# Kernel optimization log

Hardware: AMD Instinct MI355X
Metric: run time of the kernel (lower is better)

The kernel has to match this reference:

```python
import jax, jax.numpy as jnp
import numpy as np

HIDDEN = 64
IN_DIM = 32
CONNECTION = 8
N_WARPS = (CONNECTION + 1) // 2  # range(0, connection, 2) -> 4 warps actually used


def conv2d(x, w, b, pad):
    # x: (B, Cin, H, W), w: (Cout, Cin, kh, kw)
    y = jax.lax.conv_general_dilated(
        x, w, window_strides=(1, 1), padding=[(pad, pad), (pad, pad)],
        dimension_numbers=("NCHW", "OIHW", "NCHW"))
    return y + b[None, :, None, None]


def grid_sample_bilinear(img, grid):
    """torch.nn.functional.grid_sample(mode='bilinear', padding_mode='zeros', align_corners=False).
    img: (B, C, H, W); grid: (B, H, W, 2) with grid[..., 0]=x (width), grid[..., 1]=y (height)."""
    B, C, H, W = img.shape
    gx = (grid[..., 0] + 1.0) * (W * 0.5) - 0.5  # unnormalize, align_corners=False
    gy = (grid[..., 1] + 1.0) * (H * 0.5) - 0.5
    x0 = jnp.floor(gx)
    y0 = jnp.floor(gy)
    wx1 = gx - x0
    wy1 = gy - y0
    wx0 = 1.0 - wx1
    wy0 = 1.0 - wy1

    def gather(xf, yf):
        valid = (xf >= 0) & (xf < W) & (yf >= 0) & (yf < H)
        xi = jnp.clip(xf, 0, W - 1).astype(jnp.int32)
        yi = jnp.clip(yf, 0, H - 1).astype(jnp.int32)
        # per-batch advanced gather: (C, H, W) per sample
        v = jax.vmap(lambda im, y, x: im[:, y, x])(img, yi, xi)  # (B, C, H, W)
        return v * valid[:, None, :, :].astype(img.dtype)

    out = (wy0 * wx0)[:, None] * gather(x0, y0) \
        + (wy0 * wx1)[:, None] * gather(x0 + 1, y0) \
        + (wy1 * wx0)[:, None] * gather(x0, y0 + 1) \
        + (wy1 * wx1)[:, None] * gather(x0 + 1, y0 + 1)
    return out


def setup_inputs() -> dict:
    key = jax.random.key(0)
    ks = jax.random.split(key, 10)
    B, H, W = 16, 128, 128
    s = 0.05
    return {
        "x": jax.random.normal(ks[0], (B, IN_DIM, H, W), dtype=jnp.float32),
        "h_prev": jax.random.normal(ks[1], (B, HIDDEN, H, W), dtype=jnp.float32),
        "w_in": jax.random.normal(ks[2], (3 * HIDDEN, IN_DIM, 3, 3), dtype=jnp.float32) * s,
        "b_in": jax.random.normal(ks[3], (3 * HIDDEN,), dtype=jnp.float32) * s,
        "w_proj": jax.random.normal(ks[4], (N_WARPS, 3 * HIDDEN, HIDDEN), dtype=jnp.float32) * s,
        "b_proj": jax.random.normal(ks[5], (N_WARPS, 3 * HIDDEN), dtype=jnp.float32) * s,
        "w_sub": jax.random.normal(ks[6], (2 * CONNECTION, IN_DIM + HIDDEN, 5, 5), dtype=jnp.float32) * s,
        "b_sub": jax.random.normal(ks[7], (2 * CONNECTION,), dtype=jnp.float32) * s,
    }


def reference(x, h_prev, w_in, b_in, w_proj, b_proj, w_sub, b_sub):
    d = HIDDEN
    input_conv = conv2d(x, w_in, b_in, pad=1)  # (B, 3d, H, W)
    x_z, x_r, x_h = input_conv[:, :d], input_conv[:, d:2 * d], input_conv[:, 2 * d:]

    # flow sub-network + global min-max normalization over ALL channels
    combined = jnp.concatenate([x, h_prev], axis=1)
    cc = conv2d(combined, w_sub, b_sub, pad=2)  # (B, 2*connection, H, W)
    cc = jnp.transpose(cc, (0, 2, 3, 1))        # (B, H, W, 2*connection)
    cc = (cc - cc.min()) / (cc.max() - cc.min())
    cc = 2.0 * cc - 1.0

    traj = None
    for i in range(N_WARPS):  # small fixed loop (mirrors range(0, connection, 2))
        grid = cc[..., 2 * i:2 * i + 2]
        warped = grid_sample_bilinear(h_prev, grid)  # (B, d, H, W)
        proj = jnp.einsum("bchw,oc->bohw", warped, w_proj[i]) + b_proj[i][None, :, None, None]
        traj = proj if traj is None else traj + proj

    h_z, h_r, h_h = traj[:, :d], traj[:, d:2 * d], traj[:, 2 * d:]
    z = jax.nn.sigmoid(x_z + h_z)
    r = jax.nn.sigmoid(x_r + h_r)
    h = jax.nn.leaky_relu(x_h + r * h_h, negative_slope=0.2)
    h_next = (1.0 - z) * h + z * h_prev
    return h_next
```

## Files before the change

### kernel.cpp

```cpp
#include <hip/hip_runtime.h>
#include <hip/hip_bf16.h>
#include <math.h>

#define B_    16
#define HID   64
#define CIN   32
#define OC1   192
#define CCC   16
#define HW_   128
#define NPIX  (HW_*HW_)

typedef _Float16 half8 __attribute__((ext_vector_type(8)));
typedef _Float16 half4 __attribute__((ext_vector_type(4)));
typedef float floatx4 __attribute__((ext_vector_type(4)));

__device__ __forceinline__ unsigned fenc(float f) {
    unsigned b = __float_as_uint(f);
    return (b & 0x80000000u) ? ~b : (b | 0x80000000u);
}
__device__ __forceinline__ float fdec(unsigned u) {
    unsigned b = (u & 0x80000000u) ? (u ^ 0x80000000u) : ~u;
    return __uint_as_float(b);
}

__global__ __launch_bounds__(256) void repack_kernel(
    const float* __restrict__ w_in, const float* __restrict__ w_sub,
    const float* __restrict__ w_proj, const float* __restrict__ b_proj,
    _Float16* __restrict__ wsub_f16, float* __restrict__ bsum,
    _Float16* __restrict__ win_f16, _Float16* __restrict__ wp_f16,
    unsigned* __restrict__ minmax)
{
    int idx = blockIdx.x * 256 + threadIdx.x;
    if (idx < 38400) {
        int sk = idx >> 9, r2 = idx & 511;
        int l = r2 >> 3, j = r2 & 7;
        int s = sk / 3, kc = sk - s * 3;
        int ky = s / 5, kx = s - ky * 5;
        int oc = l & 15;
        int icg = kc * 32 + (l >> 4) * 8 + j;
        wsub_f16[idx] = (_Float16)w_sub[oc * 2400 + icg * 25 + ky * 5 + kx];
    } else if (idx < 38400 + 192) {
        int o = idx - 38400;
        bsum[o] = b_proj[o] + b_proj[192 + o] + b_proj[384 + o] + b_proj[576 + o];
    } else if (idx < 38592 + 55296) {
        int j2 = idx - 38592;
        int s = j2 / 6144, r = j2 - s * 6144;
        int mt = r / 512, r2 = r - mt * 512;
        int l = r2 >> 3, j = r2 & 7;
        int oc = mt * 16 + (l & 15);
        int ic = (l >> 4) * 8 + j;
        win_f16[j2] = (_Float16)w_in[oc * 288 + ic * 9 + s];
    } else if (idx < 38592 + 55296 + 49152) {
        int j3 = idx - (38592 + 55296);
        int kt = j3 / 6144, r = j3 - kt * 6144;
        int mt = r / 512, r2 = r - mt * 512;
        int l = r2 >> 3, j = r2 & 7;
        int o = mt * 16 + (l & 15);
        int c_all = kt * 32 + (l >> 4) * 8 + j;
        int i = c_all >> 6, c = c_all & 63;
        wp_f16[j3] = (_Float16)w_proj[(i * 192 + o) * 64 + c];
    }
    if (idx == 0) { minmax[0] = 0xFFFFFFFFu; minmax[1] = 0u; }
}

__global__ __launch_bounds__(256) void transpose_h_kernel(
    const float* __restrict__ hp, const float* __restrict__ x,
    _Float16* __restrict__ hcl, _Float16* __restrict__ xcl)
{
    __shared__ float lds[64 * 129];
    int tid = threadIdx.x;
    int y = blockIdx.x, b = blockIdx.y;

    const float* hb = hp + (size_t)b * HID * NPIX + y * HW_;
#pragma unroll
    for (int it = 0; it < 32; ++it) {
        int idx = tid + it * 256;
        int c = idx >> 7, xx = idx & 127;
        lds[c * 129 + xx] = hb[(size_t)c * NPIX + xx];
    }
    __syncthreads();
    unsigned* o = (unsigned*)(hcl + (size_t)((b * HW_ + y) * HW_) * 64);
#pragma unroll
    for (int it = 0; it < 16; ++it) {
        int e2 = tid + it * 256;
        int c2 = e2 & 31, xx = e2 >> 5;
        union { _Float16 h[2]; unsigned u; } pk;
        pk.h[0] = (_Float16)lds[(c2 * 2) * 129 + xx];
        pk.h[1] = (_Float16)lds[(c2 * 2 + 1) * 129 + xx];
        o[e2] = pk.u;
    }
    __syncthreads();

    const float* xb = x + (size_t)b * CIN * NPIX + y * HW_;
#pragma unroll
    for (int it = 0; it < 16; ++it) {
        int idx = tid + it * 256;
        int c = idx >> 7, xx = idx & 127;
        lds[c * 129 + xx] = xb[(size_t)c * NPIX + xx];
    }
    __syncthreads();
    unsigned* ox = (unsigned*)(xcl + (size_t)((b * HW_ + y) * HW_) * 32);
#pragma unroll
    for (int it = 0; it < 8; ++it) {
        int e2 = tid + it * 256;
        int c2 = e2 & 15, xx = e2 >> 4;
        union { _Float16 h[2]; unsigned u; } pk;
        pk.h[0] = (_Float16)lds[(c2 * 2) * 129 + xx];
        pk.h[1] = (_Float16)lds[(c2 * 2 + 1) * 129 + xx];
        ox[e2] = pk.u;
    }
}

__global__ __launch_bounds__(256) void conv_sub_mfma(
    const _Float16* __restrict__ xcl, const _Float16* __restrict__ hcl,
    const _Float16* __restrict__ wsub_f16, const float* __restrict__ b_sub,
    float* __restrict__ cc, unsigned* __restrict__ minmax)
{
    __shared__ __align__(16) _Float16 tile[12 * 20 * 104];
    __shared__ float redmn[4], redmx[4];
    int tid = threadIdx.x;
    int b = blockIdx.z;
    int y0 = blockIdx.y * 8, x0 = blockIdx.x * 16;

#pragma unroll
    for (int it = 0; it < 8; ++it) {
        int idx = tid + it * 256;
        if (idx < 1920) {
            int yy = idx / 160, rem = idx - yy * 160;
            int px = rem >> 3, q = rem & 7;
            int gy = y0 + yy - 2, gx = x0 + px - 2;
            bool ok = ((unsigned)gy < 128u) & ((unsigned)gx < 128u);
            int cgy = min(max(gy, 0), 127), cgx = min(max(gx, 0), 127);
            uint4 v = ((const uint4*)hcl)[(size_t)((b * 128 + cgy) * 128 + cgx) * 8 + q];
            if (!ok) { v.x = 0; v.y = 0; v.z = 0; v.w = 0; }
            *(uint4*)((char*)tile + (yy * 20 + px) * 208 + 64 + q * 16) = v;
        }
    }
#pragma unroll
    for (int it = 0; it < 4; ++it) {
        int idx = tid + it * 256;
        if (idx < 960) {
            int yy = idx / 80, rem = idx - yy * 80;
            int px = rem >> 2, q = rem & 3;
            int gy = y0 + yy - 2, gx = x0 + px - 2;
            bool ok = ((unsigned)gy < 128u) & ((unsigned)gx < 128u);
            int cgy = min(max(gy, 0), 127), cgx = min(max(gx, 0), 127);
            uint4 v = ((const uint4*)xcl)[(size_t)((b * 128 + cgy) * 128 + cgx) * 4 + q];
            if (!ok) { v.x = 0; v.y = 0; v.z = 0; v.w = 0; }
            *(uint4*)((char*)tile + (yy * 20 + px) * 208 + q * 16) = v;
        }
    }
    __syncthreads();

    int w = tid >> 6, l = tid & 63;
    int quad = l >> 4, ln = l & 15;

    floatx4 sinit;
#pragma unroll
    for (int r = 0; r < 4; ++r) sinit[r] = b_sub[quad * 4 + r];
    floatx4 sacc[2] = {sinit, sinit};

#pragma unroll 5
    for (int s = 0; s < 25; ++s) {
        int ky = s / 5, kx = s - (s / 5) * 5;
#pragma unroll
        for (int kc = 0; kc < 3; ++kc) {
            half8 af = *(const half8*)(wsub_f16 + (size_t)((s * 3 + kc) * 64 + l) * 8);
#pragma unroll
            for (int t = 0; t < 2; ++t) {
                int pos = (w * 2 + t + ky) * 20 + (ln + kx);
                half8 bf = *(const half8*)(tile + pos * 104 + kc * 32 + quad * 8);
                sacc[t] = __builtin_amdgcn_mfma_f32_16x16x32_f16(af, bf, sacc[t], 0, 0, 0);
            }
        }
    }

    {
        float mn = 1e30f, mx = -1e30f;
#pragma unroll
        for (int t = 0; t < 2; ++t) {
            int yg = y0 + w * 2 + t;
#pragma unroll
            for (int r = 0; r < 4; ++r) {
                int oc = quad * 4 + r;
                float v = sacc[t][r];
                cc[((size_t)(b * CCC + oc) * HW_ + yg) * HW_ + x0 + ln] = v;
                mn = fminf(mn, v); mx = fmaxf(mx, v);
            }
        }
#pragma unroll
        for (int m = 1; m < 64; m <<= 1) {
            mn = fminf(mn, __shfl_xor(mn, m, 64));
            mx = fmaxf(mx, __shfl_xor(mx, m, 64));
        }
        if (l == 0) { redmn[w] = mn; redmx[w] = mx; }
    }
    __syncthreads();
    if (tid == 0) {
        float bmn = fminf(fminf(redmn[0], redmn[1]), fminf(redmn[2], redmn[3]));
        float bmx = fmaxf(fmaxf(redmx[0], redmx[1]), fmaxf(redmx[2], redmx[3]));
        atomicMin(&minmax[0], fenc(bmn));
        atomicMax(&minmax[1], fenc(bmx));
    }
}

__global__ __launch_bounds__(256, 3) void warp_gru_conv(
    const _Float16* __restrict__ hcl, const _Float16* __restrict__ xcl,
    const float* __restrict__ cc,
    const _Float16* __restrict__ wp_f16, const float* __restrict__ bsum,
    const _Float16* __restrict__ win_f16, const float* __restrict__ b_in,
    const unsigned* __restrict__ minmax, float* __restrict__ out)
{
    __shared__ __align__(16) _Float16 smem[64 * 256];
    _Float16* xt = smem;
    _Float16* warped = smem;
    float* ol = (float*)smem;

    int tid = threadIdx.x;
    int i = tid >> 6;
    int p = tid & 63;
    int b = blockIdx.z, y = blockIdx.y, xh = blockIdx.x;
    int xg = xh * 64 + p;
    int w = i, l = p;
    int quad = l >> 4, ln = l & 15;

    uint4 xv0, xv1, xv2, xv3;
    int xslot = -1;
    if (tid < 216) {
        int row = tid / 72, px = tid - row * 72;
        int gy = y - 1 + row, gx = xh * 64 - 4 + px;
        bool ok = ((unsigned)gy < 128u) & ((unsigned)gx < 128u);
        int cgy = min(max(gy, 0), 127), cgx = min(max(gx, 0), 127);
        const uint4* s = (const uint4*)(xcl + (size_t)((b * 128 + cgy) * 128 + cgx) * 32);
        xv0 = s[0]; xv1 = s[1]; xv2 = s[2]; xv3 = s[3];
        if (!ok) {
            xv0.x = xv0.y = xv0.z = xv0.w = 0; xv1 = xv0; xv2 = xv0; xv3 = xv0;
        }
        xslot = (row * 72 + px) * 4;
    }

    const _Float16* hclb = hcl + (size_t)b * NPIX * 64;
    half4 hpv16[4];
    {
        const _Float16* grow = hclb + (size_t)(y * HW_ + xh * 64) * 64 + 16 * w + quad * 4;
#pragma unroll
        for (int nt = 0; nt < 4; ++nt)
            hpv16[nt] = *(const half4*)(grow + (size_t)(nt * 16 + ln) * 64);
    }

    float mn = fdec(minmax[0]), mx = fdec(minmax[1]);
    float scale = 2.0f / (mx - mn);
    int ccbase = ((b * CCC + 2 * i) * HW_ + y) * HW_ + xg;
    float gxn = (cc[ccbase] - mn) * scale - 1.0f;
    float gyn = (cc[ccbase + NPIX] - mn) * scale - 1.0f;
    float gx = (gxn + 1.0f) * 64.0f - 0.5f;
    float gy = (gyn + 1.0f) * 64.0f - 0.5f;
    float x0f = floorf(gx), y0f = floorf(gy);
    float wx1 = gx - x0f, wy1 = gy - y0f;
    float wx0 = 1.0f - wx1, wy0 = 1.0f - wy1;
    int ix0 = (int)x0f, iy0 = (int)y0f;
    int ix1 = ix0 + 1, iy1 = iy0 + 1;
    bool vx0 = (unsigned)ix0 < 128u, vx1 = (unsigned)ix1 < 128u;
    bool vy0 = (unsigned)iy0 < 128u, vy1 = (unsigned)iy1 < 128u;
    _Float16 h00 = (_Float16)((vx0 && vy0) ? wy0 * wx0 : 0.f);
    _Float16 h01 = (_Float16)((vx1 && vy0) ? wy0 * wx1 : 0.f);
    _Float16 h10 = (_Float16)((vx0 && vy1) ? wy1 * wx0 : 0.f);
    _Float16 h11 = (_Float16)((vx1 && vy1) ? wy1 * wx1 : 0.f);
    int cx0 = min(max(ix0, 0), 127), cx1 = min(max(ix1, 0), 127);
    int cy0 = min(max(iy0, 0), 127), cy1 = min(max(iy1, 0), 127);

    const half8* r00 = (const half8*)(hclb + (size_t)(cy0 * HW_ + cx0) * 64);
    const half8* r01 = (const half8*)(hclb + (size_t)(cy0 * HW_ + cx1) * 64);
    const half8* r10 = (const half8*)(hclb + (size_t)(cy1 * HW_ + cx0) * 64);
    const half8* r11 = (const half8*)(hclb + (size_t)(cy1 * HW_ + cx1) * 64);

    if (xslot >= 0) {
        unsigned b0 = (unsigned)(xslot * 16);
        unsigned by0_ = b0 ^ (((b0 >> 7) & 3) << 4);
        unsigned b1 = (unsigned)((xslot + 1) * 16);
        unsigned by1_ = b1 ^ (((b1 >> 7) & 3) << 4);
        unsigned b2 = (unsigned)((xslot + 2) * 16);
        unsigned by2_ = b2 ^ (((b2 >> 7) & 3) << 4);
        unsigned b3 = (unsigned)((xslot + 3) * 16);
        unsigned by3_ = b3 ^ (((b3 >> 7) & 3) << 4);
        *(uint4*)((char*)xt + by0_) = xv0;
        *(uint4*)((char*)xt + by1_) = xv1;
        *(uint4*)((char*)xt + by2_) = xv2;
        *(uint4*)((char*)xt + by3_) = xv3;
    }
    __syncthreads();

    half8 g0[8], g1[8];
#pragma unroll
    for (int t = 0; t < 8; ++t) { g0[t] = r00[t]; g1[t] = r01[t]; }

    floatx4 accA[3][4];
    floatx4 hh[4];
#pragma unroll
    for (int t = 0; t < 2; ++t) {
        floatx4 bi = *(const floatx4*)(b_in + t * 64 + 16 * w + quad * 4);
        floatx4 bs = *(const floatx4*)(bsum + t * 64 + 16 * w + quad * 4);
        floatx4 init;
#pragma unroll
        for (int r = 0; r < 4; ++r) init[r] = bi[r] + bs[r];
#pragma unroll
        for (int nt = 0; nt < 4; ++nt) accA[t][nt] = init;
    }
    {
        floatx4 bih = *(const floatx4*)(b_in + 128 + 16 * w + quad * 4);
        floatx4 bsh = *(const floatx4*)(bsum + 128 + 16 * w + quad * 4);
#pragma unroll
        for (int nt = 0; nt < 4; ++nt) { accA[2][nt] = bih; hh[nt] = bsh; }
    }

#pragma unroll
    for (int s = 0; s < 9; ++s) {
        int ky = s / 3, kx = s - ky * 3;
        half8 af[3];
#pragma unroll
        for (int t = 0; t < 3; ++t)
            af[t] = *(const half8*)(win_f16 + (size_t)((s * 12 + (t * 4 + w)) * 64 + l) * 8);
#pragma unroll
        for (int nt = 0; nt < 4; ++nt) {
            int pxr = ky * 72 + nt * 16 + ln + kx + 3;
            unsigned byte = (unsigned)(pxr * 64 + quad * 16);
            byte ^= ((byte >> 7) & 3) << 4;
            half8 bf = *(const half8*)((char*)xt + byte);
#pragma unroll
            for (int t = 0; t < 3; ++t)
                accA[t][nt] = __builtin_amdgcn_mfma_f32_16x16x32_f16(af[t], bf, accA[t][nt], 0, 0, 0);
        }
    }
    __syncthreads();

#pragma unroll
    for (int t = 0; t < 8; ++t) {
        half8 c10 = r10[t], c11 = r11[t];
        half8 v = g0[t] * h00 + g1[t] * h01 + c10 * h10 + c11 * h11;
        int cs = (i * 8 + t) ^ (p & 7);
        *(half8*)(warped + p * 256 + cs * 8) = v;
    }
    __syncthreads();

#pragma unroll
    for (int kt = 0; kt < 8; ++kt) {
        half8 af[3];
#pragma unroll
        for (int t = 0; t < 3; ++t)
            af[t] = *(const half8*)(wp_f16 + (size_t)((kt * 12 + (t * 4 + w)) * 64 + l) * 8);
#pragma unroll
        for (int nt = 0; nt < 4; ++nt) {
            int pxi = nt * 16 + ln;
            int cs = (kt * 4 + quad) ^ (pxi & 7);
            half8 bf = *(const half8*)(warped + pxi * 256 + cs * 8);
            accA[0][nt] = __builtin_amdgcn_mfma_f32_16x16x32_f16(af[0], bf, accA[0][nt], 0, 0, 0);
            accA[1][nt] = __builtin_amdgcn_mfma_f32_16x16x32_f16(af[1], bf, accA[1][nt], 0, 0, 0);
            hh[nt]      = __builtin_amdgcn_mfma_f32_16x16x32_f16(af[2], bf, hh[nt], 0, 0, 0);
        }
    }

    float gout[4][4];
#pragma unroll
    for (int nt = 0; nt < 4; ++nt) {
#pragma unroll
        for (int r = 0; r < 4; ++r) {
            float z  = 1.0f / (1.0f + __expf(-accA[0][nt][r]));
            float rg = 1.0f / (1.0f + __expf(-accA[1][nt][r]));
            float hc = accA[2][nt][r] + rg * hh[nt][r];
            hc = hc > 0.f ? hc : 0.2f * hc;
            gout[nt][r] = (1.f - z) * hc + z * (float)hpv16[nt][r];
        }
    }

    __syncthreads();
#pragma unroll
    for (int nt = 0; nt < 4; ++nt) {
#pragma unroll
        for (int r = 0; r < 4; ++r) {
            int d = 16 * w + quad * 4 + r;
            ol[d * 68 + nt * 16 + ln] = gout[nt][r];
        }
    }
    __syncthreads();
    {
        const int pixbase = y * HW_ + xh * 64;
#pragma unroll
        for (int it = 0; it < 4; ++it) {
            int idx = tid + it * 256;
            int ch = idx >> 4, p4 = idx & 15;
            floatx4 v = *(const floatx4*)&ol[ch * 68 + p4 * 4];
            *(floatx4*)&out[(size_t)(b * HID + ch) * NPIX + pixbase + p4 * 4] = v;
        }
    }
}

extern "C" void kernel_launch(void* const* d_in, const int* in_sizes, int n_in,
                              void* d_out, int out_size, void* d_ws, size_t ws_size,
                              hipStream_t stream)
{
    const float* x      = (const float*)d_in[0];
    const float* hp     = (const float*)d_in[1];
    const float* w_in   = (const float*)d_in[2];
    const float* b_in   = (const float*)d_in[3];
    const float* w_proj = (const float*)d_in[4];
    const float* b_proj = (const float*)d_in[5];
    const float* w_sub  = (const float*)d_in[6];
    const float* b_sub  = (const float*)d_in[7];
    float* out = (float*)d_out;

    char* ws = (char*)d_ws;
    float*     ccbuf    = (float*)    ws;
    unsigned*  minmax   = (unsigned*) (ws + 16777216);
    _Float16*  wsub_f16 = (_Float16*)(ws + 16777472);
    float*     bsum     = (float*)    (ws + 16854272);
    _Float16*  win_f16  = (_Float16*)(ws + 16855296);
    _Float16*  wp_f16   = (_Float16*)(ws + 16965888);
    _Float16*  hcl16    = (_Float16*)(ws + 17064192);
    _Float16*  xcl16    = (_Float16*)(ws + 50618624);

    repack_kernel<<<dim3(559), dim3(256), 0, stream>>>(
        w_in, w_sub, w_proj, b_proj, wsub_f16, bsum, win_f16, wp_f16, minmax);
    transpose_h_kernel<<<dim3(HW_, B_), dim3(256), 0, stream>>>(hp, x, hcl16, xcl16);
    conv_sub_mfma<<<dim3(8, 16, B_), dim3(256), 0, stream>>>(
        xcl16, hcl16, wsub_f16, b_sub, ccbuf, minmax);
    warp_gru_conv<<<dim3(2, HW_, B_), dim3(256), 0, stream>>>(
        hcl16, xcl16, ccbuf, wp_f16, bsum, win_f16, b_in, minmax, out);
}
```

Before: 361.7 us.

## Coalesce bilinear gather loads by sharing corner indices through LDS

Instead of each thread gathering all 64 channels of its own pixel's four corner rows, the thread computes that pixel's corner offsets and weights and stores them in shared memory. Groups of 8 lanes then cooperatively load one pixel's 128-byte channel row, so each gather instruction touches contiguous 128B segments rather than 64 scattered pixels. This is meant to cut memory transactions and cache-line waste in the warp gather. It costs 8KB of extra LDS, which may reduce occupancy, plus extra LDS reads for indices and weights.

```diff
diff --git a/kernel.cpp b/kernel.cpp
--- a/kernel.cpp
+++ b/kernel.cpp
@@ -212,6 +212,8 @@
     const unsigned* __restrict__ minmax, float* __restrict__ out)
 {
     __shared__ __align__(16) _Float16 smem[64 * 256];
+    __shared__ __align__(16) int   mrec[256 * 4];
+    __shared__ __align__(16) float mw[256 * 4];
     _Float16* xt = smem;
     _Float16* warped = smem;
     float* ol = (float*)smem;
@@ -248,31 +250,33 @@
             hpv16[nt] = *(const half4*)(grow + (size_t)(nt * 16 + ln) * 64);
     }
 
-    float mn = fdec(minmax[0]), mx = fdec(minmax[1]);
-    float scale = 2.0f / (mx - mn);
-    int ccbase = ((b * CCC + 2 * i) * HW_ + y) * HW_ + xg;
-    float gxn = (cc[ccbase] - mn) * scale - 1.0f;
-    float gyn = (cc[ccbase + NPIX] - mn) * scale - 1.0f;
-    float gx = (gxn + 1.0f) * 64.0f - 0.5f;
-    float gy = (gyn + 1.0f) * 64.0f - 0.5f;
-    float x0f = floorf(gx), y0f = floorf(gy);
-    float wx1 = gx - x0f, wy1 = gy - y0f;
-    float wx0 = 1.0f - wx1, wy0 = 1.0f - wy1;
-    int ix0 = (int)x0f, iy0 = (int)y0f;
-    int ix1 = ix0 + 1, iy1 = iy0 + 1;
-    bool vx0 = (unsigned)ix0 < 128u, vx1 = (unsigned)ix1 < 128u;
-    bool vy0 = (unsigned)iy0 < 128u, vy1 = (unsigned)iy1 < 128u;
-    _Float16 h00 = (_Float16)((vx0 && vy0) ? wy0 * wx0 : 0.f);
-    _Float16 h01 = (_Float16)((vx1 && vy0) ? wy0 * wx1 : 0.f);
-    _Float16 h10 = (_Float16)((vx0 && vy1) ? wy1 * wx0 : 0.f);
-    _Float16 h11 = (_Float16)((vx1 && vy1) ? wy1 * wx1 : 0.f);
-    int cx0 = min(max(ix0, 0), 127), cx1 = min(max(ix1, 0), 127);
-    int cy0 = min(max(iy0, 0), 127), cy1 = min(max(iy1, 0), 127);
-
-    const half8* r00 = (const half8*)(hclb + (size_t)(cy0 * HW_ + cx0) * 64);
-    const half8* r01 = (const half8*)(hclb + (size_t)(cy0 * HW_ + cx1) * 64);
-    const half8* r10 = (const half8*)(hclb + (size_t)(cy1 * HW_ + cx0) * 64);
-    const half8* r11 = (const half8*)(hclb + (size_t)(cy1 * HW_ + cx1) * 64);
+    {
+        float mn = fdec(minmax[0]), mx = fdec(minmax[1]);
+        float scale = 2.0f / (mx - mn);
+        int ccbase = ((b * CCC + 2 * i) * HW_ + y) * HW_ + xg;
+        float gxn = (cc[ccbase] - mn) * scale - 1.0f;
+        float gyn = (cc[ccbase + NPIX] - mn) * scale - 1.0f;
+        float gx = (gxn + 1.0f) * 64.0f - 0.5f;
+        float gy = (gyn + 1.0f) * 64.0f - 0.5f;
+        float x0f = floorf(gx), y0f = floorf(gy);
+        float wx1 = gx - x0f, wy1 = gy - y0f;
+        float wx0 = 1.0f - wx1, wy0 = 1.0f - wy1;
+        int ix0 = (int)x0f, iy0 = (int)y0f;
+        int ix1 = ix0 + 1, iy1 = iy0 + 1;
+        bool vx0 = (unsigned)ix0 < 128u, vx1 = (unsigned)ix1 < 128u;
+        bool vy0 = (unsigned)iy0 < 128u, vy1 = (unsigned)iy1 < 128u;
+        float w00 = (vx0 && vy0) ? wy0 * wx0 : 0.f;
+        float w01 = (vx1 && vy0) ? wy0 * wx1 : 0.f;
+        float w10 = (vx0 && vy1) ? wy1 * wx0 : 0.f;
+        float w11 = (vx1 && vy1) ? wy1 * wx1 : 0.f;
+        int cx0 = min(max(ix0, 0), 127), cx1 = min(max(ix1, 0), 127);
+        int cy0 = min(max(iy0, 0), 127), cy1 = min(max(iy1, 0), 127);
+        int* mr = &mrec[tid * 4];
+        mr[0] = cy0 * HW_ + cx0; mr[1] = cy0 * HW_ + cx1;
+        mr[2] = cy1 * HW_ + cx0; mr[3] = cy1 * HW_ + cx1;
+        float* mwp = &mw[tid * 4];
+        mwp[0] = w00; mwp[1] = w01; mwp[2] = w10; mwp[3] = w11;
+    }
 
     if (xslot >= 0) {
         unsigned b0 = (unsigned)(xslot * 16);
@@ -290,9 +294,17 @@
     }
     __syncthreads();
 
+    int sub = p >> 3;
+    int e   = p & 7;
     half8 g0[8], g1[8];
 #pragma unroll
-    for (int t = 0; t < 8; ++t) { g0[t] = r00[t]; g1[t] = r01[t]; }
+    for (int it = 0; it < 8; ++it) {
+        int pp = it * 8 + sub;
+        const int* mr = &mrec[(i * 64 + pp) * 4];
+        int r0 = mr[0], r1 = mr[1];
+        g0[it] = *(const half8*)(hclb + (size_t)r0 * 64 + e * 8);
+        g1[it] = *(const half8*)(hclb + (size_t)r1 * 64 + e * 8);
+    }
 
     floatx4 accA[3][4];
     floatx4 hh[4];
@@ -334,11 +346,20 @@
     __syncthreads();
 
 #pragma unroll
-    for (int t = 0; t < 8; ++t) {
-        half8 c10 = r10[t], c11 = r11[t];
-        half8 v = g0[t] * h00 + g1[t] * h01 + c10 * h10 + c11 * h11;
-        int cs = (i * 8 + t) ^ (p & 7);
-        *(half8*)(warped + p * 256 + cs * 8) = v;
+    for (int it = 0; it < 8; ++it) {
+        int pp = it * 8 + sub;
+        const int* mr = &mrec[(i * 64 + pp) * 4];
+        const float* mwp = &mw[(i * 64 + pp) * 4];
+        int r2 = mr[2], r3 = mr[3];
+        _Float16 f00 = (_Float16)mwp[0];
+        _Float16 f01 = (_Float16)mwp[1];
+        _Float16 f10 = (_Float16)mwp[2];
+        _Float16 f11 = (_Float16)mwp[3];
+        half8 c10 = *(const half8*)(hclb + (size_t)r2 * 64 + e * 8);
+        half8 c11 = *(const half8*)(hclb + (size_t)r3 * 64 + e * 8);
+        half8 v = g0[it] * f00 + g1[it] * f01 + c10 * f10 + c11 * f11;
+        int cs = (i * 8 + e) ^ sub;
+        *(half8*)(warped + pp * 256 + cs * 8) = v;
     }
     __syncthreads();
 
```

New measurement: 379.9 us. 1.05x slower.
